# Kernel tuning notes

Measured on AMD Instinct MI355X. Metric: run time of the kernel, lower is better.

The kernel has to match this reference:

```python
import jax, jax.numpy as jnp
import numpy as np

N = 100000      # physical-network nodes
E = 3200000     # directed edges (avg degree 32)
DIN = 128       # input_dim
DH = 128        # embedding_dim
DOUT = 128      # output_dim
NUM_GRAPHS = 1


def setup_inputs() -> dict:
    key = jax.random.key(0)
    ks = jax.random.split(key, 8)
    s = 0.05
    x = jax.random.normal(ks[0], (N, DIN), dtype=jnp.float32)
    edge_index = jax.random.randint(ks[1], (2, E), 0, N, dtype=jnp.int64)
    W1 = jax.random.normal(ks[2], (DIN, DH), dtype=jnp.float32) * s
    b1 = jnp.zeros((DH,), dtype=jnp.float32)
    W2 = jax.random.normal(ks[3], (DH, DH), dtype=jnp.float32) * s
    b2 = jnp.zeros((DH,), dtype=jnp.float32)
    W3 = jax.random.normal(ks[4], (DH, DOUT), dtype=jnp.float32) * s
    b3 = jnp.zeros((DOUT,), dtype=jnp.float32)
    return {"x": x, "edge_index": edge_index,
            "W1": W1, "b1": b1, "W2": W2, "b2": b2, "W3": W3, "b3": b3}


def _gcn_norm(edge_index, n_nodes):
    # PyG GCNConv default: add self-loops, symmetric D^{-1/2} (A+I) D^{-1/2} norm.
    loops = jnp.arange(n_nodes, dtype=edge_index.dtype)
    src = jnp.concatenate([edge_index[0], loops])   # [E+N]
    dst = jnp.concatenate([edge_index[1], loops])   # [E+N]
    deg = jax.ops.segment_sum(jnp.ones_like(dst, dtype=jnp.float32), dst,
                              num_segments=n_nodes)
    dinv = jax.lax.rsqrt(deg)  # deg >= 1 because of self-loops
    norm = dinv[src] * dinv[dst]                    # [E+N]
    return src, dst, norm


def _gcn_conv(h, W, b, src, dst, norm, n_nodes):
    h = h @ W                                       # [N, dout] linear first (PyG order)
    msg = h[src] * norm[:, None]                    # gather + edge scaling
    agg = jax.ops.segment_sum(msg, dst, num_segments=n_nodes)  # scatter-add
    return agg + b


def reference(x, edge_index, W1, b1, W2, b2, W3, b3):
    src, dst, norm = _gcn_norm(edge_index, N)
    h = jax.nn.relu(_gcn_conv(x, W1, b1, src, dst, norm, N))
    # dropout is identity in eval mode
    h = jax.nn.relu(_gcn_conv(h, W2, b2, src, dst, norm, N))
    h = _gcn_conv(h, W3, b3, src, dst, norm, N)
    return h.reshape(NUM_GRAPHS, N // NUM_GRAPHS, -1)
```

## Files before the change

### kernel.cpp

```cpp
#include <hip/hip_runtime.h>
#include <cstddef>
#include <cstdint>

#define NN 100000
#define NE 3200000
#define D  128
#define NB 782
#define BSH 7
#define NPB 512
#define CHUNK 6250
#define BCAP 4608

typedef short v8s __attribute__((ext_vector_type(8)));
typedef float v4f __attribute__((ext_vector_type(4)));


__device__ __forceinline__ unsigned short f2bf(float f) {
  uint32_t u = __float_as_uint(f);
  uint32_t r = u + 0x7fff + ((u >> 16) & 1);
  return (unsigned short)(r >> 16);
}
__device__ __forceinline__ float bf_lo(uint32_t v) {
  return __uint_as_float(v << 16);
}
__device__ __forceinline__ float bf_hi(uint32_t v) {
  return __uint_as_float(v & 0xffff0000u);
}


__global__ __launch_bounds__(256) void kb_part2(const int* __restrict__ src,
                                                const int* __restrict__ dst,
                                                int* __restrict__ gcur,
                                                uint32_t* __restrict__ ebuf) {
  __shared__ int h[NB];
  __shared__ int cur[NB];
  for (int i = threadIdx.x; i < NB; i += 256) h[i] = 0;
  __syncthreads();
  int lo = blockIdx.x * CHUNK, hi = lo + CHUNK;
  if (hi > NE) hi = NE;
  for (int e = lo + threadIdx.x; e < hi; e += 256)
    atomicAdd(&h[dst[e] >> BSH], 1);
  __syncthreads();
  for (int i = threadIdx.x; i < NB; i += 256)
    cur[i] = h[i] ? atomicAdd(&gcur[i], h[i]) : 0;
  __syncthreads();
  for (int e = lo + threadIdx.x; e < hi; e += 256) {
    int s = src[e], d = dst[e];
    int b = d >> BSH;
    int p = atomicAdd(&cur[b], 1);
    if (p < BCAP)
      ebuf[(size_t)b * BCAP + p] = ((uint32_t)s << BSH) | (uint32_t)(d & 127);
  }
}

__global__ __launch_bounds__(256) void kb_build(const uint32_t* __restrict__ ebuf,
                                                const int* __restrict__ gcur,
                                                int* __restrict__ row_off,
                                                int* __restrict__ row_end,
                                                float* __restrict__ dinv,
                                                int* __restrict__ col) {
  int b = blockIdx.x;
  __shared__ int h[128];
  __shared__ int s[128];
  __shared__ int cur[128];
  if (threadIdx.x < 128) h[threadIdx.x] = 0;
  __syncthreads();
  const uint32_t* eb = ebuf + (size_t)b * BCAP;
  int cnt = gcur[b];
  for (int e = threadIdx.x; e < cnt; e += 256)
    atomicAdd(&h[eb[e] & 127], 1);
  __syncthreads();
  int v = (threadIdx.x < 128) ? h[threadIdx.x] : 0;
  if (threadIdx.x < 128) s[threadIdx.x] = v;
  __syncthreads();
  for (int d = 1; d < 128; d <<= 1) {
    int t = (threadIdx.x < 128 && threadIdx.x >= d) ? s[threadIdx.x - d] : 0;
    __syncthreads();
    if (threadIdx.x < 128) s[threadIdx.x] += t;
    __syncthreads();
  }
  if (threadIdx.x < 128) {
    int ro = b * BCAP + s[threadIdx.x] - v;
    cur[threadIdx.x] = ro;
    int node = b * 128 + threadIdx.x;
    if (node < NN) {
      row_off[node] = ro;
      row_end[node] = ro + v;
      dinv[node] = rsqrtf((float)(v + 1));
    }
  }
  __syncthreads();
  for (int e = threadIdx.x; e < cnt; e += 256) {
    uint32_t p = eb[e];
    int pos = atomicAdd(&cur[p & 127], 1);
    col[pos] = (int)(p >> BSH);
  }
}


__global__ void k_wt3z(const float* __restrict__ W1, const float* __restrict__ W2,
                       const float* __restrict__ W3, unsigned short* __restrict__ wt,
                       int* __restrict__ gcur) {
  int idx = blockIdx.x * 256 + threadIdx.x;
  if (idx < NB) gcur[idx] = 0;
  if (idx >= 3 * 16384) return;
  int m = idx >> 14, rem = idx & 16383;
  int k = rem >> 7, c = rem & 127;
  const float* W = (m == 0) ? W1 : (m == 1) ? W2 : W3;
  wt[m * 16384 + c * 128 + k] = f2bf(W[rem]);
}


__global__ __launch_bounds__(128) void k_gemm2(const float* __restrict__ A,
                                               const unsigned short* __restrict__ wt,
                                               const float* __restrict__ dinv,
                                               unsigned short* __restrict__ C) {
  const int wave = threadIdx.x >> 6;
  const int lane = threadIdx.x & 63;
  const int row0 = blockIdx.x * 128 + wave * 64;
  const int rl = lane & 15;
  const int kg = lane >> 4;

  v4f acc[4][8];
#pragma unroll
  for (int t = 0; t < 4; ++t)
#pragma unroll
    for (int ct = 0; ct < 8; ++ct) acc[t][ct] = (v4f){0.f, 0.f, 0.f, 0.f};

  union U { uint4 u; v8s v; unsigned short us[8]; };

#pragma unroll
  for (int ks = 0; ks < 4; ++ks) {
    U a[4];
#pragma unroll
    for (int t = 0; t < 4; ++t) {
      int r = row0 + t * 16 + rl;
      if (r >= NN) r = NN - 1;
      const float* ap = A + (size_t)r * D + ks * 32 + kg * 8;
      float4 l4 = *(const float4*)ap;
      float4 h4 = *(const float4*)(ap + 4);
      a[t].us[0] = f2bf(l4.x); a[t].us[1] = f2bf(l4.y);
      a[t].us[2] = f2bf(l4.z); a[t].us[3] = f2bf(l4.w);
      a[t].us[4] = f2bf(h4.x); a[t].us[5] = f2bf(h4.y);
      a[t].us[6] = f2bf(h4.z); a[t].us[7] = f2bf(h4.w);
    }
#pragma unroll
    for (int ct = 0; ct < 8; ++ct) {
      U b;
      b.u = *(const uint4*)(wt + (size_t)(ct * 16 + rl) * 128 + ks * 32 + kg * 8);
#pragma unroll
      for (int t = 0; t < 4; ++t)
        acc[t][ct] =
            __builtin_amdgcn_mfma_f32_16x16x32_bf16(a[t].v, b.v, acc[t][ct], 0, 0, 0);
    }
  }

#pragma unroll
  for (int t = 0; t < 4; ++t) {
#pragma unroll
    for (int i = 0; i < 4; ++i) {
      int row = row0 + t * 16 + kg * 4 + i;
      if (row < NN) {
        float dv = dinv[row];
#pragma unroll
        for (int ct = 0; ct < 8; ++ct)
          C[(size_t)row * D + ct * 16 + rl] = f2bf(dv * acc[t][ct][i]);
      }
    }
  }
}


#define AGG8(e0, q0, q1)                                     \
  {                                                          \
    int s0 = col[e0], s1 = col[e0 + 1], s2 = col[e0 + 2],    \
        s3 = col[e0 + 3], s4 = col[e0 + 4], s5 = col[e0 + 5],\
        s6 = col[e0 + 6], s7 = col[e0 + 7];                  \
    uint32_t v0 = tu[(size_t)s0 * 64 + lane];                \
    uint32_t v1 = tu[(size_t)s1 * 64 + lane];                \
    uint32_t v2 = tu[(size_t)s2 * 64 + lane];                \
    uint32_t v3 = tu[(size_t)s3 * 64 + lane];                \
    uint32_t v4 = tu[(size_t)s4 * 64 + lane];                \
    uint32_t v5 = tu[(size_t)s5 * 64 + lane];                \
    uint32_t v6 = tu[(size_t)s6 * 64 + lane];                \
    uint32_t v7 = tu[(size_t)s7 * 64 + lane];                \
    q0 += bf_lo(v0); q1 += bf_hi(v0);                        \
    q0 += bf_lo(v1); q1 += bf_hi(v1);                        \
    q0 += bf_lo(v2); q1 += bf_hi(v2);                        \
    q0 += bf_lo(v3); q1 += bf_hi(v3);                        \
    q0 += bf_lo(v4); q1 += bf_hi(v4);                        \
    q0 += bf_lo(v5); q1 += bf_hi(v5);                        \
    q0 += bf_lo(v6); q1 += bf_hi(v6);                        \
    q0 += bf_lo(v7); q1 += bf_hi(v7);                        \
  }

#define GATHER_BODY()                                                        \
  uint32_t svA = tu[(size_t)gA * 64 + lane];                                 \
  uint32_t svB = tu[(size_t)gB * 64 + lane];                                 \
  float a0 = bf_lo(svA), a1 = bf_hi(svA);                                    \
  float b0 = bf_lo(svB), b1 = bf_hi(svB);                                    \
  int eA = row_off[gA], endA = row_end[gA];                                  \
  int eB = row_off[gB], endB = row_end[gB];                                  \
  while (eA + 8 <= endA && eB + 8 <= endB) {                                 \
    int sA0 = col[eA],     sA1 = col[eA + 1], sA2 = col[eA + 2],             \
        sA3 = col[eA + 3], sA4 = col[eA + 4], sA5 = col[eA + 5],             \
        sA6 = col[eA + 6], sA7 = col[eA + 7];                                \
    int sB0 = col[eB],     sB1 = col[eB + 1], sB2 = col[eB + 2],             \
        sB3 = col[eB + 3], sB4 = col[eB + 4], sB5 = col[eB + 5],             \
        sB6 = col[eB + 6], sB7 = col[eB + 7];                                \
    uint32_t vA0 = tu[(size_t)sA0 * 64 + lane];                              \
    uint32_t vA1 = tu[(size_t)sA1 * 64 + lane];                              \
    uint32_t vA2 = tu[(size_t)sA2 * 64 + lane];                              \
    uint32_t vA3 = tu[(size_t)sA3 * 64 + lane];                              \
    uint32_t vA4 = tu[(size_t)sA4 * 64 + lane];                              \
    uint32_t vA5 = tu[(size_t)sA5 * 64 + lane];                              \
    uint32_t vA6 = tu[(size_t)sA6 * 64 + lane];                              \
    uint32_t vA7 = tu[(size_t)sA7 * 64 + lane];                              \
    uint32_t vB0 = tu[(size_t)sB0 * 64 + lane];                              \
    uint32_t vB1 = tu[(size_t)sB1 * 64 + lane];                              \
    uint32_t vB2 = tu[(size_t)sB2 * 64 + lane];                              \
    uint32_t vB3 = tu[(size_t)sB3 * 64 + lane];                              \
    uint32_t vB4 = tu[(size_t)sB4 * 64 + lane];                              \
    uint32_t vB5 = tu[(size_t)sB5 * 64 + lane];                              \
    uint32_t vB6 = tu[(size_t)sB6 * 64 + lane];                              \
    uint32_t vB7 = tu[(size_t)sB7 * 64 + lane];                              \
    a0 += bf_lo(vA0); a1 += bf_hi(vA0);                                      \
    a0 += bf_lo(vA1); a1 += bf_hi(vA1);                                      \
    a0 += bf_lo(vA2); a1 += bf_hi(vA2);                                      \
    a0 += bf_lo(vA3); a1 += bf_hi(vA3);                                      \
    a0 += bf_lo(vA4); a1 += bf_hi(vA4);                                      \
    a0 += bf_lo(vA5); a1 += bf_hi(vA5);                                      \
    a0 += bf_lo(vA6); a1 += bf_hi(vA6);                                      \
    a0 += bf_lo(vA7); a1 += bf_hi(vA7);                                      \
    b0 += bf_lo(vB0); b1 += bf_hi(vB0);                                      \
    b0 += bf_lo(vB1); b1 += bf_hi(vB1);                                      \
    b0 += bf_lo(vB2); b1 += bf_hi(vB2);                                      \
    b0 += bf_lo(vB3); b1 += bf_hi(vB3);                                      \
    b0 += bf_lo(vB4); b1 += bf_hi(vB4);                                      \
    b0 += bf_lo(vB5); b1 += bf_hi(vB5);                                      \
    b0 += bf_lo(vB6); b1 += bf_hi(vB6);                                      \
    b0 += bf_lo(vB7); b1 += bf_hi(vB7);                                      \
    eA += 8; eB += 8;                                                        \
  }                                                                          \
  for (; eA + 8 <= endA; eA += 8) AGG8(eA, a0, a1);                          \
  for (; eA < endA; ++eA) {                                                  \
    uint32_t v = tu[(size_t)col[eA] * 64 + lane];                            \
    a0 += bf_lo(v); a1 += bf_hi(v);                                          \
  }                                                                          \
  for (; eB + 8 <= endB; eB += 8) AGG8(eB, b0, b1);                          \
  for (; eB < endB; ++eB) {                                                  \
    uint32_t v = tu[(size_t)col[eB] * 64 + lane];                            \
    b0 += bf_lo(v); b1 += bf_hi(v);                                          \
  }


__global__ __launch_bounds__(128) void k_aggf(
    const uint32_t* __restrict__ tu, const int* __restrict__ row_off,
    const int* __restrict__ row_end, const int* __restrict__ col,
    const float* __restrict__ dinv, const float* __restrict__ bias,
    const unsigned short* __restrict__ wt, unsigned short* __restrict__ t_out) {
  const int wave = threadIdx.x >> 6;
  const int lane = threadIdx.x & 63;
  const int base = blockIdx.x * 32 + wave * 16;

  __shared__ uint32_t lds[2][16 * 64];
  uint32_t* lw = lds[wave];

  const int c = lane * 2;
  const float bl = bias[c], bh = bias[c + 1];

#pragma unroll 1
  for (int p = 0; p < 8; ++p) {
    int gA = base + 2 * p;
    int gB = gA + 1;
    if (gA >= NN) gA = NN - 1;
    if (gB >= NN) gB = NN - 1;
    const float diA = dinv[gA], diB = dinv[gB];

    GATHER_BODY();

    uint32_t packA = (uint32_t)f2bf(fmaxf(diA * a0 + bl, 0.f)) |
                     ((uint32_t)f2bf(fmaxf(diA * a1 + bh, 0.f)) << 16);
    uint32_t packB = (uint32_t)f2bf(fmaxf(diB * b0 + bl, 0.f)) |
                     ((uint32_t)f2bf(fmaxf(diB * b1 + bh, 0.f)) << 16);
    const int rA = 2 * p, rB = rA + 1;
    lw[rA * 64 + (lane ^ ((rA & 7) << 2))] = packA;
    lw[rB * 64 + (lane ^ ((rB & 7) << 2))] = packB;
  }

  const int rl = lane & 15;
  const int kg = lane >> 4;
  union U { uint4 u; v8s v; };

  float di4[4];
#pragma unroll
  for (int i = 0; i < 4; ++i) {
    int node = base + kg * 4 + i;
    di4[i] = dinv[node < NN ? node : NN - 1];
  }

#pragma unroll
  for (int ct = 0; ct < 8; ++ct) {
    v4f acc = (v4f){0.f, 0.f, 0.f, 0.f};
#pragma unroll
    for (int ks = 0; ks < 4; ++ks) {
      U a, b;
      a.u = *(const uint4*)&lw[rl * 64 + ((ks * 16 + kg * 4) ^ ((rl & 7) << 2))];
      b.u = *(const uint4*)(wt + (size_t)(ct * 16 + rl) * 128 + ks * 32 + kg * 8);
      acc = __builtin_amdgcn_mfma_f32_16x16x32_bf16(a.v, b.v, acc, 0, 0, 0);
    }
#pragma unroll
    for (int i = 0; i < 4; ++i) {
      int node = base + kg * 4 + i;
      if (node < NN)
        t_out[(size_t)node * D + ct * 16 + rl] = f2bf(di4[i] * acc[i]);
    }
  }
}


__global__ __launch_bounds__(256) void k_agg2(
    const uint32_t* __restrict__ tu, const int* __restrict__ row_off,
    const int* __restrict__ row_end, const int* __restrict__ col,
    const float* __restrict__ dinv, const float* __restrict__ bias,
    float* __restrict__ outf) {
  const int wave = threadIdx.x >> 6;
  const int lane = threadIdx.x & 63;
  const int gA = blockIdx.x * 8 + wave * 2;
  const int gB = gA + 1;

  const float diA = dinv[gA], diB = dinv[gB];

  GATHER_BODY();

  int c = lane * 2;
  float rA0 = diA * a0 + bias[c];
  float rA1 = diA * a1 + bias[c + 1];
  float rB0 = diB * b0 + bias[c];
  float rB1 = diB * b1 + bias[c + 1];
  *(float2*)(outf + (size_t)gA * D + c) = make_float2(rA0, rA1);
  *(float2*)(outf + (size_t)gB * D + c) = make_float2(rB0, rB1);
}


extern "C" void kernel_launch(void* const* d_in, const int* in_sizes, int n_in,
                              void* d_out, int out_size, void* d_ws, size_t ws_size,
                              hipStream_t stream) {
  const float* x  = (const float*)d_in[0];
  const int*   ei = (const int*)d_in[1];
  const float* W1 = (const float*)d_in[2];
  const float* b1 = (const float*)d_in[3];
  const float* W2 = (const float*)d_in[4];
  const float* b2 = (const float*)d_in[5];
  const float* W3 = (const float*)d_in[6];
  const float* b3 = (const float*)d_in[7];
  float* out = (float*)d_out;

  char* base = (char*)d_ws;
  size_t o = 0;
  auto take = [&](size_t bytes) {
    void* p = base + o;
    o += (bytes + 255) & ~(size_t)255;
    return p;
  };
  int*   row_off = (int*)take((size_t)NN * 4);
  int*   row_end = (int*)take((size_t)NN * 4);
  float* dinv    = (float*)take((size_t)NN * 4);
  int*   gcur    = (int*)take((size_t)NB * 4);
  unsigned short* wt = (unsigned short*)take(3 * 16384 * 2);
  void* region1 = take((size_t)NN * D * 2);
  int*  col     = (int*)take((size_t)NB * BCAP * 4);
  unsigned short* t0 = (unsigned short*)take((size_t)NN * D * 2);

  uint32_t* ebuf = (uint32_t*)region1;
  unsigned short* t1 = (unsigned short*)region1;

  const int* src = ei;
  const int* dst = ei + NE;

  k_wt3z  <<<192, 256, 0, stream>>>(W1, W2, W3, wt, gcur);
  kb_part2<<<NPB, 256, 0, stream>>>(src, dst, gcur, ebuf);
  kb_build<<<NB, 256, 0, stream>>>(ebuf, gcur, row_off, row_end, dinv, col);

  const int gB = (NN + 127) / 128;
  const int fB = (NN + 31) / 32;
  const int aB = NN / 8;

  k_gemm2<<<gB, 128, 0, stream>>>(x, wt, dinv, t0);
  k_aggf<<<fB, 128, 0, stream>>>((const uint32_t*)t0, row_off, row_end, col, dinv,
                                 b1, wt + 16384, t1);
  k_aggf<<<fB, 128, 0, stream>>>((const uint32_t*)t1, row_off, row_end, col, dinv,
                                 b2, wt + 32768, t0);
  k_agg2<<<aB, 256, 0, stream>>>((const uint32_t*)t0, row_off, row_end, col, dinv,
                                 b3, out);
}
```

Baseline: 477.7 us.

## Split wave into half-waves gathering two rows, each covering half the features

Reworks the gather so lanes 0-31 serve node A and lanes 32-63 serve node B. Each half-wave loads 128-byte row segments, and the feature dimension is covered in two passes. A single load instruction now fetches two different neighbour rows, halving the per-lane accumulator state and the number of independent loads per edge batch. In exchange the edge index list is walked twice and accesses are narrower per row, and the tail loops run with predicated zero adds, so unequal degrees waste lanes.

```diff
diff --git a/kernel.cpp b/kernel.cpp
--- a/kernel.cpp
+++ b/kernel.cpp
@@ -171,86 +171,74 @@
 }
 
 
-#define AGG8(e0, q0, q1)                                     \
-  {                                                          \
-    int s0 = col[e0], s1 = col[e0 + 1], s2 = col[e0 + 2],    \
-        s3 = col[e0 + 3], s4 = col[e0 + 4], s5 = col[e0 + 5],\
-        s6 = col[e0 + 6], s7 = col[e0 + 7];                  \
-    uint32_t v0 = tu[(size_t)s0 * 64 + lane];                \
-    uint32_t v1 = tu[(size_t)s1 * 64 + lane];                \
-    uint32_t v2 = tu[(size_t)s2 * 64 + lane];                \
-    uint32_t v3 = tu[(size_t)s3 * 64 + lane];                \
-    uint32_t v4 = tu[(size_t)s4 * 64 + lane];                \
-    uint32_t v5 = tu[(size_t)s5 * 64 + lane];                \
-    uint32_t v6 = tu[(size_t)s6 * 64 + lane];                \
-    uint32_t v7 = tu[(size_t)s7 * 64 + lane];                \
-    q0 += bf_lo(v0); q1 += bf_hi(v0);                        \
-    q0 += bf_lo(v1); q1 += bf_hi(v1);                        \
-    q0 += bf_lo(v2); q1 += bf_hi(v2);                        \
-    q0 += bf_lo(v3); q1 += bf_hi(v3);                        \
-    q0 += bf_lo(v4); q1 += bf_hi(v4);                        \
-    q0 += bf_lo(v5); q1 += bf_hi(v5);                        \
-    q0 += bf_lo(v6); q1 += bf_hi(v6);                        \
-    q0 += bf_lo(v7); q1 += bf_hi(v7);                        \
-  }
-
-#define GATHER_BODY()                                                        \
-  uint32_t svA = tu[(size_t)gA * 64 + lane];                                 \
-  uint32_t svB = tu[(size_t)gB * 64 + lane];                                 \
-  float a0 = bf_lo(svA), a1 = bf_hi(svA);                                    \
-  float b0 = bf_lo(svB), b1 = bf_hi(svB);                                    \
-  int eA = row_off[gA], endA = row_end[gA];                                  \
-  int eB = row_off[gB], endB = row_end[gB];                                  \
-  while (eA + 8 <= endA && eB + 8 <= endB) {                                 \
-    int sA0 = col[eA],     sA1 = col[eA + 1], sA2 = col[eA + 2],             \
-        sA3 = col[eA + 3], sA4 = col[eA + 4], sA5 = col[eA + 5],             \
-        sA6 = col[eA + 6], sA7 = col[eA + 7];                                \
-    int sB0 = col[eB],     sB1 = col[eB + 1], sB2 = col[eB + 2],             \
-        sB3 = col[eB + 3], sB4 = col[eB + 4], sB5 = col[eB + 5],             \
-        sB6 = col[eB + 6], sB7 = col[eB + 7];                                \
-    uint32_t vA0 = tu[(size_t)sA0 * 64 + lane];                              \
-    uint32_t vA1 = tu[(size_t)sA1 * 64 + lane];                              \
-    uint32_t vA2 = tu[(size_t)sA2 * 64 + lane];                              \
-    uint32_t vA3 = tu[(size_t)sA3 * 64 + lane];                              \
-    uint32_t vA4 = tu[(size_t)sA4 * 64 + lane];                              \
-    uint32_t vA5 = tu[(size_t)sA5 * 64 + lane];                              \
-    uint32_t vA6 = tu[(size_t)sA6 * 64 + lane];                              \
-    uint32_t vA7 = tu[(size_t)sA7 * 64 + lane];                              \
-    uint32_t vB0 = tu[(size_t)sB0 * 64 + lane];                              \
-    uint32_t vB1 = tu[(size_t)sB1 * 64 + lane];                              \
-    uint32_t vB2 = tu[(size_t)sB2 * 64 + lane];                              \
-    uint32_t vB3 = tu[(size_t)sB3 * 64 + lane];                              \
-    uint32_t vB4 = tu[(size_t)sB4 * 64 + lane];                              \
-    uint32_t vB5 = tu[(size_t)sB5 * 64 + lane];                              \
-    uint32_t vB6 = tu[(size_t)sB6 * 64 + lane];                              \
-    uint32_t vB7 = tu[(size_t)sB7 * 64 + lane];                              \
-    a0 += bf_lo(vA0); a1 += bf_hi(vA0);                                      \
-    a0 += bf_lo(vA1); a1 += bf_hi(vA1);                                      \
-    a0 += bf_lo(vA2); a1 += bf_hi(vA2);                                      \
-    a0 += bf_lo(vA3); a1 += bf_hi(vA3);                                      \
-    a0 += bf_lo(vA4); a1 += bf_hi(vA4);                                      \
-    a0 += bf_lo(vA5); a1 += bf_hi(vA5);                                      \
-    a0 += bf_lo(vA6); a1 += bf_hi(vA6);                                      \
-    a0 += bf_lo(vA7); a1 += bf_hi(vA7);                                      \
-    b0 += bf_lo(vB0); b1 += bf_hi(vB0);                                      \
-    b0 += bf_lo(vB1); b1 += bf_hi(vB1);                                      \
-    b0 += bf_lo(vB2); b1 += bf_hi(vB2);                                      \
-    b0 += bf_lo(vB3); b1 += bf_hi(vB3);                                      \
-    b0 += bf_lo(vB4); b1 += bf_hi(vB4);                                      \
-    b0 += bf_lo(vB5); b1 += bf_hi(vB5);                                      \
-    b0 += bf_lo(vB6); b1 += bf_hi(vB6);                                      \
-    b0 += bf_lo(vB7); b1 += bf_hi(vB7);                                      \
-    eA += 8; eB += 8;                                                        \
-  }                                                                          \
-  for (; eA + 8 <= endA; eA += 8) AGG8(eA, a0, a1);                          \
-  for (; eA < endA; ++eA) {                                                  \
-    uint32_t v = tu[(size_t)col[eA] * 64 + lane];                            \
-    a0 += bf_lo(v); a1 += bf_hi(v);                                          \
-  }                                                                          \
-  for (; eB + 8 <= endB; eB += 8) AGG8(eB, b0, b1);                          \
-  for (; eB < endB; ++eB) {                                                  \
-    uint32_t v = tu[(size_t)col[eB] * 64 + lane];                            \
-    b0 += bf_lo(v); b1 += bf_hi(v);                                          \
+#define DUAL8(eAi, eBi)                                                      \
+  {                                                                          \
+    int sA0 = col[eAi],     sA1 = col[eAi + 1], sA2 = col[eAi + 2],          \
+        sA3 = col[eAi + 3], sA4 = col[eAi + 4], sA5 = col[eAi + 5],          \
+        sA6 = col[eAi + 6], sA7 = col[eAi + 7];                              \
+    int sB0 = col[eBi],     sB1 = col[eBi + 1], sB2 = col[eBi + 2],          \
+        sB3 = col[eBi + 3], sB4 = col[eBi + 4], sB5 = col[eBi + 5],          \
+        sB6 = col[eBi + 6], sB7 = col[eBi + 7];                              \
+    uint32_t v0 = tu[(size_t)(lo32 ? sA0 : sB0) * 64 + h32l];                \
+    uint32_t v1 = tu[(size_t)(lo32 ? sA1 : sB1) * 64 + h32l];                \
+    uint32_t v2 = tu[(size_t)(lo32 ? sA2 : sB2) * 64 + h32l];                \
+    uint32_t v3 = tu[(size_t)(lo32 ? sA3 : sB3) * 64 + h32l];                \
+    uint32_t v4 = tu[(size_t)(lo32 ? sA4 : sB4) * 64 + h32l];                \
+    uint32_t v5 = tu[(size_t)(lo32 ? sA5 : sB5) * 64 + h32l];                \
+    uint32_t v6 = tu[(size_t)(lo32 ? sA6 : sB6) * 64 + h32l];                \
+    uint32_t v7 = tu[(size_t)(lo32 ? sA7 : sB7) * 64 + h32l];                \
+    q0 += bf_lo(v0); q1 += bf_hi(v0);                                        \
+    q0 += bf_lo(v1); q1 += bf_hi(v1);                                        \
+    q0 += bf_lo(v2); q1 += bf_hi(v2);                                        \
+    q0 += bf_lo(v3); q1 += bf_hi(v3);                                        \
+    q0 += bf_lo(v4); q1 += bf_hi(v4);                                        \
+    q0 += bf_lo(v5); q1 += bf_hi(v5);                                        \
+    q0 += bf_lo(v6); q1 += bf_hi(v6);                                        \
+    q0 += bf_lo(v7); q1 += bf_hi(v7);                                        \
+  }
+
+#define DRAIN8(e0, pred)                                                     \
+  {                                                                          \
+    int s0 = col[e0], s1 = col[e0 + 1], s2 = col[e0 + 2], s3 = col[e0 + 3],  \
+        s4 = col[e0 + 4], s5 = col[e0 + 5], s6 = col[e0 + 6], s7 = col[e0 + 7];\
+    uint32_t v0 = tu[(size_t)s0 * 64 + h32l];                                \
+    uint32_t v1 = tu[(size_t)s1 * 64 + h32l];                                \
+    uint32_t v2 = tu[(size_t)s2 * 64 + h32l];                                \
+    uint32_t v3 = tu[(size_t)s3 * 64 + h32l];                                \
+    uint32_t v4 = tu[(size_t)s4 * 64 + h32l];                                \
+    uint32_t v5 = tu[(size_t)s5 * 64 + h32l];                                \
+    uint32_t v6 = tu[(size_t)s6 * 64 + h32l];                                \
+    uint32_t v7 = tu[(size_t)s7 * 64 + h32l];                                \
+    q0 += (pred) ? bf_lo(v0) : 0.f; q1 += (pred) ? bf_hi(v0) : 0.f;          \
+    q0 += (pred) ? bf_lo(v1) : 0.f; q1 += (pred) ? bf_hi(v1) : 0.f;          \
+    q0 += (pred) ? bf_lo(v2) : 0.f; q1 += (pred) ? bf_hi(v2) : 0.f;          \
+    q0 += (pred) ? bf_lo(v3) : 0.f; q1 += (pred) ? bf_hi(v3) : 0.f;          \
+    q0 += (pred) ? bf_lo(v4) : 0.f; q1 += (pred) ? bf_hi(v4) : 0.f;          \
+    q0 += (pred) ? bf_lo(v5) : 0.f; q1 += (pred) ? bf_hi(v5) : 0.f;          \
+    q0 += (pred) ? bf_lo(v6) : 0.f; q1 += (pred) ? bf_hi(v6) : 0.f;          \
+    q0 += (pred) ? bf_lo(v7) : 0.f; q1 += (pred) ? bf_hi(v7) : 0.f;          \
+  }
+
+#define DRAIN1(e0, pred)                                                     \
+  {                                                                          \
+    uint32_t v = tu[(size_t)col[e0] * 64 + h32l];                            \
+    q0 += (pred) ? bf_lo(v) : 0.f; q1 += (pred) ? bf_hi(v) : 0.f;            \
+  }
+
+#define GATHER_HALF()                                                        \
+  float q0, q1;                                                              \
+  {                                                                          \
+    uint32_t sv = tu[(size_t)gMy * 64 + h32l];                               \
+    q0 = bf_lo(sv); q1 = bf_hi(sv);                                          \
+    int eA = roA, eB = roB;                                                  \
+    while (eA + 8 <= endA && eB + 8 <= endB) {                               \
+      DUAL8(eA, eB);                                                         \
+      eA += 8; eB += 8;                                                      \
+    }                                                                        \
+    for (; eA + 8 <= endA; eA += 8) DRAIN8(eA, lo32);                        \
+    for (; eA < endA; ++eA) DRAIN1(eA, lo32);                                \
+    for (; eB + 8 <= endB; eB += 8) DRAIN8(eB, !lo32);                       \
+    for (; eB < endB; ++eB) DRAIN1(eB, !lo32);                               \
   }
 
 
@@ -261,13 +249,12 @@
     const unsigned short* __restrict__ wt, unsigned short* __restrict__ t_out) {
   const int wave = threadIdx.x >> 6;
   const int lane = threadIdx.x & 63;
+  const bool lo32 = lane < 32;
+  const int l31 = lane & 31;
   const int base = blockIdx.x * 32 + wave * 16;
 
   __shared__ uint32_t lds[2][16 * 64];
   uint32_t* lw = lds[wave];
-
-  const int c = lane * 2;
-  const float bl = bias[c], bh = bias[c + 1];
 
 #pragma unroll 1
   for (int p = 0; p < 8; ++p) {
@@ -275,17 +262,22 @@
     int gB = gA + 1;
     if (gA >= NN) gA = NN - 1;
     if (gB >= NN) gB = NN - 1;
-    const float diA = dinv[gA], diB = dinv[gB];
-
-    GATHER_BODY();
-
-    uint32_t packA = (uint32_t)f2bf(fmaxf(diA * a0 + bl, 0.f)) |
-                     ((uint32_t)f2bf(fmaxf(diA * a1 + bh, 0.f)) << 16);
-    uint32_t packB = (uint32_t)f2bf(fmaxf(diB * b0 + bl, 0.f)) |
-                     ((uint32_t)f2bf(fmaxf(diB * b1 + bh, 0.f)) << 16);
-    const int rA = 2 * p, rB = rA + 1;
-    lw[rA * 64 + (lane ^ ((rA & 7) << 2))] = packA;
-    lw[rB * 64 + (lane ^ ((rB & 7) << 2))] = packB;
+    const int gMy = lo32 ? gA : gB;
+    const float dMy = dinv[gMy];
+    const int roA = row_off[gA], endA = row_end[gA];
+    const int roB = row_off[gB], endB = row_end[gB];
+    const int r = 2 * p + (lo32 ? 0 : 1);
+
+#pragma unroll 1
+    for (int h = 0; h < 2; ++h) {
+      const int h32l = h * 32 + l31;
+      GATHER_HALF();
+      int cc = h * 64 + 2 * l31;
+      float r0 = fmaxf(dMy * q0 + bias[cc], 0.f);
+      float r1 = fmaxf(dMy * q1 + bias[cc + 1], 0.f);
+      uint32_t pk = (uint32_t)f2bf(r0) | ((uint32_t)f2bf(r1) << 16);
+      lw[r * 64 + (h32l ^ ((r & 7) << 2))] = pk;
+    }
   }
 
   const int rl = lane & 15;
@@ -326,20 +318,24 @@
     float* __restrict__ outf) {
   const int wave = threadIdx.x >> 6;
   const int lane = threadIdx.x & 63;
+  const bool lo32 = lane < 32;
+  const int l31 = lane & 31;
   const int gA = blockIdx.x * 8 + wave * 2;
   const int gB = gA + 1;
-
-  const float diA = dinv[gA], diB = dinv[gB];
-
-  GATHER_BODY();
-
-  int c = lane * 2;
-  float rA0 = diA * a0 + bias[c];
-  float rA1 = diA * a1 + bias[c + 1];
-  float rB0 = diB * b0 + bias[c];
-  float rB1 = diB * b1 + bias[c + 1];
-  *(float2*)(outf + (size_t)gA * D + c) = make_float2(rA0, rA1);
-  *(float2*)(outf + (size_t)gB * D + c) = make_float2(rB0, rB1);
+  const int gMy = lo32 ? gA : gB;
+  const float dMy = dinv[gMy];
+  const int roA = row_off[gA], endA = row_end[gA];
+  const int roB = row_off[gB], endB = row_end[gB];
+
+#pragma unroll 1
+  for (int h = 0; h < 2; ++h) {
+    const int h32l = h * 32 + l31;
+    GATHER_HALF();
+    int cc = h * 64 + 2 * l31;
+    float r0 = dMy * q0 + bias[cc];
+    float r1 = dMy * q1 + bias[cc + 1];
+    *(float2*)(outf + (size_t)gMy * D + cc) = make_float2(r0, r1);
+  }
 }
 
 
```

New measurement: 602.0 us. 26.0% more time.
